# Kernel tuning notes

Measured on AMD Instinct MI355X. Metric: run time of the kernel, lower is better.

The kernel has to match this reference:

```python
import jax, jax.numpy as jnp
import numpy as np

G = 7          # grid_size
A = 2          # anchors_per_cell
C = 3          # num_classes
L_COORD, L_OBJ, L_NOOBJ, L_CLS = 5.0, 1.0, 0.5, 2.0


def setup_inputs() -> dict:
    key = jax.random.key(0)
    k0, k1, k2, k3, k4 = jax.random.split(key, 5)
    B, M = 32768, 20
    predictions = jax.random.normal(k0, (B, G, G, A, 5 + C), dtype=jnp.float32)
    xy1 = jax.random.uniform(k1, (B, M, 2), dtype=jnp.float32) * 0.8
    wh = jax.random.uniform(k2, (B, M, 2), dtype=jnp.float32) * 0.19 + 0.01
    target_boxes = jnp.concatenate([xy1, xy1 + wh], axis=-1)  # valid x1<x2, y1<y2
    target_labels = jax.random.randint(k3, (B, M), 0, C, dtype=jnp.int32)
    num_objs = jax.random.randint(k4, (B,), 0, M + 1, dtype=jnp.int32)
    anchors = jnp.array([[0.971, 1.7338], [3.4579, 5.1653]], dtype=jnp.float32)
    class_weights = jnp.array([1.0, 4.9, 4.8], dtype=jnp.float32)
    return dict(predictions=predictions, target_boxes=target_boxes,
                target_labels=target_labels, num_objs=num_objs,
                anchors=anchors, class_weights=class_weights)


def assign_targets(target_boxes, target_labels, num_objs, anchors, B):
    """Vectorized scatter-based replacement of the nested python assignment loop."""
    M = target_boxes.shape[1]
    x1, y1, x2, y2 = [target_boxes[..., i] for i in range(4)]  # (B,M)
    cx, cy = (x1 + x2) * 0.5, (y1 + y2) * 0.5
    w, h = x2 - x1, y2 - y1
    valid = (w > 0) & (h > 0) & (jnp.arange(M)[None, :] < num_objs[:, None])
    gi = jnp.clip(jnp.floor(cy * G).astype(jnp.int32), 0, G - 1)
    gj = jnp.clip(jnp.floor(cx * G).astype(jnp.int32), 0, G - 1)
    wg, hg = w * G, h * G
    # anchor matching IoU (width/height only), (B,M,A)
    inter = jnp.minimum(wg[..., None], anchors[:, 0]) * jnp.minimum(hg[..., None], anchors[:, 1])
    union = (wg * hg)[..., None] + anchors[:, 0] * anchors[:, 1] - inter
    best_a = jnp.argmax(inter / (union + 1e-6), axis=-1).astype(jnp.int32)  # first max = torch loop tie-break
    aw = anchors[best_a, 0]
    ah = anchors[best_a, 1]
    tx = cx * G - gj.astype(jnp.float32)
    ty = cy * G - gi.astype(jnp.float32)
    tw = jnp.log(jnp.clip(wg, 0.01, None) / (aw + 1e-6))
    th = jnp.log(jnp.clip(hg, 0.01, None) / (ah + 1e-6))
    tvals = jnp.stack([tx, ty, tw, th], axis=-1)  # (B,M,4)
    N = B * G * G * A
    bidx = jnp.arange(B, dtype=jnp.int32)[:, None]
    flat = ((bidx * G + gi) * G + gj) * A + best_a  # (B,M)
    flat = jnp.where(valid, flat, N)                # invalid -> dropped by scatter
    idx = flat.ravel()
    obj_mask = jnp.zeros((N,), jnp.float32).at[idx].set(1.0, mode='drop')
    target_bbox = jnp.zeros((N, 4), jnp.float32).at[idx].set(tvals.reshape(-1, 4), mode='drop')
    target_cls = jnp.zeros((N,), jnp.int32).at[idx].set(target_labels.ravel(), mode='drop')
    shape = (B, G, G, A)
    return obj_mask.reshape(shape), target_bbox.reshape(shape + (4,)), target_cls.reshape(shape)


def reference(predictions, target_boxes, target_labels, num_objs, anchors, class_weights):
    B = predictions.shape[0]
    pred_obj = predictions[..., 0]
    pred_bbox = predictions[..., 1:5]
    pred_cls = predictions[..., 5:]
    m, target_bbox, target_cls = assign_targets(target_boxes, target_labels, num_objs, anchors, B)
    sp = jax.nn.softplus
    # BCE-with-logits: target is 1 on obj cells, 0 on noobj cells
    loss_obj = jnp.sum(m * sp(-pred_obj))
    loss_noobj = jnp.sum((1.0 - m) * sp(pred_obj))
    # smooth L1 (beta=1), summed over obj cells
    d = pred_bbox - target_bbox
    ad = jnp.abs(d)
    sl1 = jnp.where(ad < 1.0, 0.5 * d * d, ad - 0.5)
    loss_bbox = jnp.sum(m[..., None] * sl1)
    # weighted cross entropy on obj cells
    logZ = jax.nn.logsumexpimport if False else jax.scipy.special.logsumexp(pred_cls, axis=-1)
    logit_t = jnp.take_along_axis(pred_cls, target_cls[..., None], axis=-1)[..., 0]
    loss_cls = jnp.sum(m * class_weights[target_cls] * (logZ - logit_t))
    num_pos = jnp.maximum(jnp.sum(m), 1.0)
    total = (L_COORD * loss_bbox + L_OBJ * loss_obj + L_NOOBJ * loss_noobj + L_CLS * loss_cls) / num_pos
    return total
```

## Files before the change

kernel.cpp:

```cpp
#include <hip/hip_runtime.h>


namespace {
constexpr int kG = 7;
constexpr int kA = 2;
constexpr int kM = 20;
constexpr int kCells = kG * kG * kA;
constexpr int kCh = 8;
constexpr int kNB = 32;
constexpr int kBlockA = 448;
constexpr int kTgt = kNB * kM;
constexpr int kBlockN = 256;
constexpr int kGridN = 2048;
}

__device__ __forceinline__ float softplus_fast(float x) {
    return fmaxf(x, 0.0f) + __logf(1.0f + __expf(-fabsf(x)));
}

__global__ __launch_bounds__(kBlockA) void det_loss_assign(
    const float* __restrict__ preds,
    const float* __restrict__ tboxes,
    const int* __restrict__ tlabels,
    const int* __restrict__ nobjs,
    const float* __restrict__ anchors,
    const float* __restrict__ cweights,
    float* __restrict__ partial,
    int B, int NT)
{
    __shared__ float4 s_tv[kTgt];
    __shared__ short  s_cell[kTgt];
    __shared__ int    s_pos[kTgt];
    __shared__ int    s_nobj[kNB];
    __shared__ int    s_npos;
    __shared__ float  s_red[kBlockA / 64][4];

    const int tid = threadIdx.x;
    const int b0 = blockIdx.x * kNB;

    if (tid < kNB) {
        const int b = b0 + tid;
        s_nobj[tid] = (b < B) ? nobjs[b] : 0;
    }
    if (tid == 0) s_npos = 0;
    __syncthreads();

    const float a00 = anchors[0], a01 = anchors[1];
    const float a10 = anchors[2], a11 = anchors[3];

    for (int j = tid; j < kTgt; j += kBlockA) {
        const int bl = j / kM;
        const int m  = j - bl * kM;
        short cell = -1;
        float4 tv = make_float4(0.f, 0.f, 0.f, 0.f);
        if (b0 + bl < B) {
            const float4 box = ((const float4*)tboxes)[(size_t)b0 * kM + j];
            const float x1 = box.x, y1 = box.y, x2 = box.z, y2 = box.w;
            const float cx = (x1 + x2) * 0.5f, cy = (y1 + y2) * 0.5f;
            const float w = x2 - x1, h = y2 - y1;
            if (w > 0.f && h > 0.f && m < s_nobj[bl]) {
                const int gi = min(max((int)floorf(cy * (float)kG), 0), kG - 1);
                const int gj = min(max((int)floorf(cx * (float)kG), 0), kG - 1);
                const float wg = w * (float)kG, hg = h * (float)kG;
                const float i0 = fminf(wg, a00) * fminf(hg, a01);
                const float u0 = wg * hg + a00 * a01 - i0;
                const float r0 = i0 / (u0 + 1e-6f);
                const float i1 = fminf(wg, a10) * fminf(hg, a11);
                const float u1 = wg * hg + a10 * a11 - i1;
                const float r1 = i1 / (u1 + 1e-6f);
                const int a = (r1 > r0) ? 1 : 0;
                const float aw = a ? a10 : a00;
                const float ah = a ? a11 : a01;
                tv.x = cx * (float)kG - (float)gj;
                tv.y = cy * (float)kG - (float)gi;
                tv.z = __logf(fmaxf(wg, 0.01f) / (aw + 1e-6f));
                tv.w = __logf(fmaxf(hg, 0.01f) / (ah + 1e-6f));
                cell = (short)(bl * kCells + (gi * kG + gj) * kA + a);
            }
        }
        s_cell[j] = cell;
        s_tv[j] = tv;
    }
    __syncthreads();

    for (int j = tid; j < kTgt; j += kBlockA) {
        const short c = s_cell[j];
        if (c >= 0) {
            const int bl = j / kM;
            const int m  = j - bl * kM;
            bool win = true;
            for (int m2 = m + 1; m2 < kM; ++m2) {
                if (s_cell[bl * kM + m2] == c) { win = false; break; }
            }
            if (win) {
                const int idx = atomicAdd(&s_npos, 1);
                s_pos[idx] = (j << 16) | (int)c;
            }
        }
    }
    __syncthreads();

    float accO = 0.f, accN = 0.f, accB = 0.f, accC = 0.f;
    const float* __restrict__ pblk = preds + (size_t)b0 * kCells * kCh;
    const int np = s_npos;
    const float cw0 = cweights[0], cw1 = cweights[1], cw2 = cweights[2];
    for (int t = tid; t < np; t += kBlockA) {
        const int pk = s_pos[t];
        const int j  = pk >> 16;
        const int ci = pk & 0xFFFF;
        const float4* pc = (const float4*)(pblk + (size_t)ci * kCh);
        const float4 p0 = pc[0];
        const float4 p1 = pc[1];
        const float spp = softplus_fast(p0.x);
        accN -= spp;
        accO += spp - p0.x;
        const float4 tv = s_tv[j];
        float d, ad;
        d = p0.y - tv.x; ad = fabsf(d); accB += (ad < 1.f) ? 0.5f * d * d : ad - 0.5f;
        d = p0.z - tv.y; ad = fabsf(d); accB += (ad < 1.f) ? 0.5f * d * d : ad - 0.5f;
        d = p0.w - tv.z; ad = fabsf(d); accB += (ad < 1.f) ? 0.5f * d * d : ad - 0.5f;
        d = p1.x - tv.w; ad = fabsf(d); accB += (ad < 1.f) ? 0.5f * d * d : ad - 0.5f;
        const int lab = tlabels[(size_t)b0 * kM + j];
        const float c0 = p1.y, c1 = p1.z, c2 = p1.w;
        const float mx = fmaxf(c0, fmaxf(c1, c2));
        const float lse = mx + __logf(__expf(c0 - mx) + __expf(c1 - mx) + __expf(c2 - mx));
        const float logit = (lab == 0) ? c0 : ((lab == 1) ? c1 : c2);
        const float cwv   = (lab == 0) ? cw0 : ((lab == 1) ? cw1 : cw2);
        accC += cwv * (lse - logit);
    }

    float vals[4] = {accO, accN, accB, accC};
    #pragma unroll
    for (int k = 0; k < 4; ++k) {
        float v = vals[k];
        #pragma unroll
        for (int off = 32; off > 0; off >>= 1) v += __shfl_down(v, off, 64);
        vals[k] = v;
    }
    const int wave = tid >> 6;
    const int lane = tid & 63;
    if (lane == 0) {
        #pragma unroll
        for (int k = 0; k < 4; ++k) s_red[wave][k] = vals[k];
    }
    __syncthreads();
    if (tid == 0) {
        #pragma unroll
        for (int k = 0; k < 4; ++k) {
            float t = 0.f;
            #pragma unroll
            for (int w = 0; w < kBlockA / 64; ++w) t += s_red[w][k];
            partial[(size_t)k * NT + blockIdx.x] = t;
        }
        partial[(size_t)4 * NT + blockIdx.x] = (float)np;
    }
}

__global__ __launch_bounds__(kBlockN) void det_loss_noobj(
    const float4* __restrict__ preds4,
    float* __restrict__ partial,
    long long n4, int NT, int col0)
{
    __shared__ float s_red[kBlockN / 64];
    const int tid = threadIdx.x;
    const long long gtid = (long long)blockIdx.x * kBlockN + tid;
    const long long stride = (long long)gridDim.x * kBlockN;
    const bool hasObj = ((gtid & 1) == 0);
    float acc = 0.f;
    long long i = gtid;
    for (; i + 3 * stride < n4; i += 4 * stride) {
        const float4 v0 = preds4[i];
        const float4 v1 = preds4[i + stride];
        const float4 v2 = preds4[i + 2 * stride];
        const float4 v3 = preds4[i + 3 * stride];
        if (hasObj) {
            acc += softplus_fast(v0.x);
            acc += softplus_fast(v1.x);
            acc += softplus_fast(v2.x);
            acc += softplus_fast(v3.x);
        }
    }
    for (; i < n4; i += stride) {
        const float4 v = preds4[i];
        if (hasObj) acc += softplus_fast(v.x);
    }

    #pragma unroll
    for (int off = 32; off > 0; off >>= 1) acc += __shfl_down(acc, off, 64);
    if ((tid & 63) == 0) s_red[tid >> 6] = acc;
    __syncthreads();
    if (tid == 0) {
        float t = 0.f;
        #pragma unroll
        for (int w = 0; w < kBlockN / 64; ++w) t += s_red[w];
        const int col = col0 + blockIdx.x;
        partial[(size_t)0 * NT + col] = 0.f;
        partial[(size_t)1 * NT + col] = t;
        partial[(size_t)2 * NT + col] = 0.f;
        partial[(size_t)3 * NT + col] = 0.f;
        partial[(size_t)4 * NT + col] = 0.f;
    }
}

__global__ __launch_bounds__(256) void det_loss_reduce(
    const float* __restrict__ partial, int NT, float* __restrict__ out)
{
    __shared__ float s_red[4][5];
    const int tid = threadIdx.x;
    float v[5] = {0.f, 0.f, 0.f, 0.f, 0.f};
    for (int i = tid; i < NT; i += 256) {
        #pragma unroll
        for (int k = 0; k < 5; ++k) v[k] += partial[(size_t)k * NT + i];
    }
    #pragma unroll
    for (int k = 0; k < 5; ++k) {
        float x = v[k];
        #pragma unroll
        for (int off = 32; off > 0; off >>= 1) x += __shfl_down(x, off, 64);
        v[k] = x;
    }
    const int wave = tid >> 6;
    const int lane = tid & 63;
    if (lane == 0) {
        #pragma unroll
        for (int k = 0; k < 5; ++k) s_red[wave][k] = v[k];
    }
    __syncthreads();
    if (tid == 0) {
        float t[5];
        #pragma unroll
        for (int k = 0; k < 5; ++k) {
            float s = 0.f;
            #pragma unroll
            for (int w = 0; w < 4; ++w) s += s_red[w][k];
            t[k] = s;
        }
        const float npv = fmaxf(t[4], 1.0f);
        out[0] = (5.0f * t[2] + 1.0f * t[0] + 0.5f * t[1] + 2.0f * t[3]) / npv;
    }
}

extern "C" void kernel_launch(void* const* d_in, const int* in_sizes, int n_in,
                              void* d_out, int out_size, void* d_ws, size_t ws_size,
                              hipStream_t stream) {
    const float* preds    = (const float*)d_in[0];
    const float* tboxes   = (const float*)d_in[1];
    const int*   tlabels  = (const int*)d_in[2];
    const int*   nobjs    = (const int*)d_in[3];
    const float* anchors  = (const float*)d_in[4];
    const float* cweights = (const float*)d_in[5];
    float* out = (float*)d_out;
    float* partial = (float*)d_ws;

    const int B = in_sizes[0] / (kCells * kCh);
    const int blocksA = (B + kNB - 1) / kNB;
    const int NT = blocksA + kGridN;
    const long long n4 = (long long)B * kCells * 2;

    det_loss_assign<<<blocksA, kBlockA, 0, stream>>>(
        preds, tboxes, tlabels, nobjs, anchors, cweights, partial, B, NT);
    det_loss_noobj<<<kGridN, kBlockN, 0, stream>>>(
        (const float4*)preds, partial, n4, NT, blocksA);
    det_loss_reduce<<<1, 256, 0, stream>>>(partial, NT, out);
}
```

Baseline: 186.9 us.

## Map one wave per batch item with shuffle-based dedup and nontemporal loads

After: 187.7 us. About the same (+0.4%).

```diff
diff --git a/kernel.cpp b/kernel.cpp
--- a/kernel.cpp
+++ b/kernel.cpp
@@ -7,20 +7,21 @@
 constexpr int kM = 20;
 constexpr int kCells = kG * kG * kA;
 constexpr int kCh = 8;
-constexpr int kNB = 32;
-constexpr int kBlockA = 448;
-constexpr int kTgt = kNB * kM;
+constexpr int kWavesA = 8;
+constexpr int kBlockA = 64 * kWavesA;
 constexpr int kBlockN = 256;
 constexpr int kGridN = 2048;
 }
 
+typedef float f32x4 __attribute__((ext_vector_type(4)));
+
 __device__ __forceinline__ float softplus_fast(float x) {
     return fmaxf(x, 0.0f) + __logf(1.0f + __expf(-fabsf(x)));
 }
 
 __global__ __launch_bounds__(kBlockA) void det_loss_assign(
     const float* __restrict__ preds,
-    const float* __restrict__ tboxes,
+    const float4* __restrict__ tboxes4,
     const int* __restrict__ tlabels,
     const int* __restrict__ nobjs,
     const float* __restrict__ anchors,
@@ -28,105 +29,76 @@
     float* __restrict__ partial,
     int B, int NT)
 {
-    __shared__ float4 s_tv[kTgt];
-    __shared__ short  s_cell[kTgt];
-    __shared__ int    s_pos[kTgt];
-    __shared__ int    s_nobj[kNB];
-    __shared__ int    s_npos;
-    __shared__ float  s_red[kBlockA / 64][4];
-
-    const int tid = threadIdx.x;
-    const int b0 = blockIdx.x * kNB;
-
-    if (tid < kNB) {
-        const int b = b0 + tid;
-        s_nobj[tid] = (b < B) ? nobjs[b] : 0;
-    }
-    if (tid == 0) s_npos = 0;
-    __syncthreads();
+    __shared__ float s_red[kWavesA][5];
+
+    const int tid  = threadIdx.x;
+    const int wave = tid >> 6;
+    const int m    = tid & 63;
+    const int wb   = blockIdx.x * kWavesA + wave;
+    const bool active = (wb < B);
 
     const float a00 = anchors[0], a01 = anchors[1];
     const float a10 = anchors[2], a11 = anchors[3];
 
-    for (int j = tid; j < kTgt; j += kBlockA) {
-        const int bl = j / kM;
-        const int m  = j - bl * kM;
-        short cell = -1;
-        float4 tv = make_float4(0.f, 0.f, 0.f, 0.f);
-        if (b0 + bl < B) {
-            const float4 box = ((const float4*)tboxes)[(size_t)b0 * kM + j];
-            const float x1 = box.x, y1 = box.y, x2 = box.z, y2 = box.w;
-            const float cx = (x1 + x2) * 0.5f, cy = (y1 + y2) * 0.5f;
-            const float w = x2 - x1, h = y2 - y1;
-            if (w > 0.f && h > 0.f && m < s_nobj[bl]) {
-                const int gi = min(max((int)floorf(cy * (float)kG), 0), kG - 1);
-                const int gj = min(max((int)floorf(cx * (float)kG), 0), kG - 1);
-                const float wg = w * (float)kG, hg = h * (float)kG;
-                const float i0 = fminf(wg, a00) * fminf(hg, a01);
-                const float u0 = wg * hg + a00 * a01 - i0;
-                const float r0 = i0 / (u0 + 1e-6f);
-                const float i1 = fminf(wg, a10) * fminf(hg, a11);
-                const float u1 = wg * hg + a10 * a11 - i1;
-                const float r1 = i1 / (u1 + 1e-6f);
-                const int a = (r1 > r0) ? 1 : 0;
-                const float aw = a ? a10 : a00;
-                const float ah = a ? a11 : a01;
-                tv.x = cx * (float)kG - (float)gj;
-                tv.y = cy * (float)kG - (float)gi;
-                tv.z = __logf(fmaxf(wg, 0.01f) / (aw + 1e-6f));
-                tv.w = __logf(fmaxf(hg, 0.01f) / (ah + 1e-6f));
-                cell = (short)(bl * kCells + (gi * kG + gj) * kA + a);
-            }
-        }
-        s_cell[j] = cell;
-        s_tv[j] = tv;
-    }
-    __syncthreads();
-
-    for (int j = tid; j < kTgt; j += kBlockA) {
-        const short c = s_cell[j];
-        if (c >= 0) {
-            const int bl = j / kM;
-            const int m  = j - bl * kM;
-            bool win = true;
-            for (int m2 = m + 1; m2 < kM; ++m2) {
-                if (s_cell[bl * kM + m2] == c) { win = false; break; }
-            }
-            if (win) {
-                const int idx = atomicAdd(&s_npos, 1);
-                s_pos[idx] = (j << 16) | (int)c;
-            }
-        }
-    }
-    __syncthreads();
+    int nob = 0;
+    if (active && m == 0) nob = nobjs[wb];
+    nob = __shfl(nob, 0, 64);
+
+    int cell = -1;
+    float4 tv = make_float4(0.f, 0.f, 0.f, 0.f);
+    if (active && m < kM) {
+        const float4 box = tboxes4[(size_t)wb * kM + m];
+        const float x1 = box.x, y1 = box.y, x2 = box.z, y2 = box.w;
+        const float cx = (x1 + x2) * 0.5f, cy = (y1 + y2) * 0.5f;
+        const float w = x2 - x1, h = y2 - y1;
+        if (w > 0.f && h > 0.f && m < nob) {
+            const int gi = min(max((int)floorf(cy * (float)kG), 0), kG - 1);
+            const int gj = min(max((int)floorf(cx * (float)kG), 0), kG - 1);
+            const float wg = w * (float)kG, hg = h * (float)kG;
+            const float i0 = fminf(wg, a00) * fminf(hg, a01);
+            const float u0 = wg * hg + a00 * a01 - i0;
+            const float r0 = i0 / (u0 + 1e-6f);
+            const float i1 = fminf(wg, a10) * fminf(hg, a11);
+            const float u1 = wg * hg + a10 * a11 - i1;
+            const float r1 = i1 / (u1 + 1e-6f);
+            const int a = (r1 > r0) ? 1 : 0;
+            const float aw = a ? a10 : a00;
+            const float ah = a ? a11 : a01;
+            tv.x = cx * (float)kG - (float)gj;
+            tv.y = cy * (float)kG - (float)gi;
+            tv.z = __logf(fmaxf(wg, 0.01f) / (aw + 1e-6f));
+            tv.w = __logf(fmaxf(hg, 0.01f) / (ah + 1e-6f));
+            cell = (gi * kG + gj) * kA + a;
+        }
+    }
+
+    bool win = (cell >= 0);
+    #pragma unroll
+    for (int s = 1; s < kM; ++s) {
+        const int other = __shfl_down(cell, s, 64);
+        if ((m + s < kM) && (cell >= 0) && (other == cell)) win = false;
+    }
+    const unsigned long long bal = __ballot(win);
 
     float accO = 0.f, accN = 0.f, accB = 0.f, accC = 0.f;
-    const float* __restrict__ pblk = preds + (size_t)b0 * kCells * kCh;
-    const int np = s_npos;
-    const float cw0 = cweights[0], cw1 = cweights[1], cw2 = cweights[2];
-    for (int t = tid; t < np; t += kBlockA) {
-        const int pk = s_pos[t];
-        const int j  = pk >> 16;
-        const int ci = pk & 0xFFFF;
-        const float4* pc = (const float4*)(pblk + (size_t)ci * kCh);
+    if (win) {
+        const float4* pc = (const float4*)(preds + ((size_t)wb * kCells + cell) * kCh);
         const float4 p0 = pc[0];
         const float4 p1 = pc[1];
         const float spp = softplus_fast(p0.x);
         accN -= spp;
         accO += spp - p0.x;
-        const float4 tv = s_tv[j];
         float d, ad;
         d = p0.y - tv.x; ad = fabsf(d); accB += (ad < 1.f) ? 0.5f * d * d : ad - 0.5f;
         d = p0.z - tv.y; ad = fabsf(d); accB += (ad < 1.f) ? 0.5f * d * d : ad - 0.5f;
         d = p0.w - tv.z; ad = fabsf(d); accB += (ad < 1.f) ? 0.5f * d * d : ad - 0.5f;
         d = p1.x - tv.w; ad = fabsf(d); accB += (ad < 1.f) ? 0.5f * d * d : ad - 0.5f;
-        const int lab = tlabels[(size_t)b0 * kM + j];
+        const int lab = tlabels[(size_t)wb * kM + m];
         const float c0 = p1.y, c1 = p1.z, c2 = p1.w;
         const float mx = fmaxf(c0, fmaxf(c1, c2));
         const float lse = mx + __logf(__expf(c0 - mx) + __expf(c1 - mx) + __expf(c2 - mx));
         const float logit = (lab == 0) ? c0 : ((lab == 1) ? c1 : c2);
-        const float cwv   = (lab == 0) ? cw0 : ((lab == 1) ? cw1 : cw2);
-        accC += cwv * (lse - logit);
+        accC += cweights[lab] * (lse - logit);
     }
 
     float vals[4] = {accO, accN, accB, accC};
@@ -137,27 +109,30 @@
         for (int off = 32; off > 0; off >>= 1) v += __shfl_down(v, off, 64);
         vals[k] = v;
     }
-    const int wave = tid >> 6;
-    const int lane = tid & 63;
-    if (lane == 0) {
+    if (m == 0) {
         #pragma unroll
         for (int k = 0; k < 4; ++k) s_red[wave][k] = vals[k];
+        s_red[wave][4] = (float)__popcll(bal);
     }
     __syncthreads();
+
     if (tid == 0) {
-        #pragma unroll
-        for (int k = 0; k < 4; ++k) {
-            float t = 0.f;
+        float t[5];
+        #pragma unroll
+        for (int k = 0; k < 5; ++k) {
+            float s = 0.f;
             #pragma unroll
-            for (int w = 0; w < kBlockA / 64; ++w) t += s_red[w][k];
-            partial[(size_t)k * NT + blockIdx.x] = t;
-        }
-        partial[(size_t)4 * NT + blockIdx.x] = (float)np;
+            for (int w = 0; w < kWavesA; ++w) s += s_red[w][k];
+            t[k] = s;
+        }
+        #pragma unroll
+        for (int k = 0; k < 5; ++k)
+            partial[(size_t)k * NT + blockIdx.x] = t[k];
     }
 }
 
 __global__ __launch_bounds__(kBlockN) void det_loss_noobj(
-    const float4* __restrict__ preds4,
+    const f32x4* __restrict__ preds4,
     float* __restrict__ partial,
     long long n4, int NT, int col0)
 {
@@ -169,10 +144,10 @@
     float acc = 0.f;
     long long i = gtid;
     for (; i + 3 * stride < n4; i += 4 * stride) {
-        const float4 v0 = preds4[i];
-        const float4 v1 = preds4[i + stride];
-        const float4 v2 = preds4[i + 2 * stride];
-        const float4 v3 = preds4[i + 3 * stride];
+        const f32x4 v0 = __builtin_nontemporal_load(preds4 + i);
+        const f32x4 v1 = __builtin_nontemporal_load(preds4 + i + stride);
+        const f32x4 v2 = __builtin_nontemporal_load(preds4 + i + 2 * stride);
+        const f32x4 v3 = __builtin_nontemporal_load(preds4 + i + 3 * stride);
         if (hasObj) {
             acc += softplus_fast(v0.x);
             acc += softplus_fast(v1.x);
@@ -181,7 +156,7 @@
         }
     }
     for (; i < n4; i += stride) {
-        const float4 v = preds4[i];
+        const f32x4 v = __builtin_nontemporal_load(preds4 + i);
         if (hasObj) acc += softplus_fast(v.x);
     }
 
@@ -253,13 +228,14 @@
     float* partial = (float*)d_ws;
 
     const int B = in_sizes[0] / (kCells * kCh);
-    const int blocksA = (B + kNB - 1) / kNB;
+    const int blocksA = (B + kWavesA - 1) / kWavesA;
     const int NT = blocksA + kGridN;
     const long long n4 = (long long)B * kCells * 2;
 
     det_loss_assign<<<blocksA, kBlockA, 0, stream>>>(
-        preds, tboxes, tlabels, nobjs, anchors, cweights, partial, B, NT);
+        preds, (const float4*)tboxes, tlabels, nobjs, anchors, cweights,
+        partial, B, NT);
     det_loss_noobj<<<kGridN, kBlockN, 0, stream>>>(
-        (const float4*)preds, partial, n4, NT, blocksA);
+        (const f32x4*)preds, partial, n4, NT, blocksA);
     det_loss_reduce<<<1, 256, 0, stream>>>(partial, NT, out);
 }
```
